# Kernel tuning notes

Measured on AMD Instinct MI355X. Metric: run time of the kernel, lower is better.

Reference implementation:

```python
import jax, jax.numpy as jnp
import numpy as np

N = 2048

def setup_inputs() -> dict:
    key = jax.random.key(0)
    k0, k1, k2, k3 = jax.random.split(key, 4)
    return {
        "input": jax.random.normal(k0, (N, N), dtype=jnp.float32),
        "weight1": jax.random.normal(k1, (N, N), dtype=jnp.float32),
        "weight2": jax.random.normal(k2, (N, N), dtype=jnp.float32),
        "weight3": jax.random.normal(k3, (N, N), dtype=jnp.float32),
    }

def reference(input, weight1, weight2, weight3):
    # Faithful translation of the torch DAG (duplicate mm kept: t4 == t2,
    # so t8 is mathematically zero, but we preserve the original math).
    t1 = input @ weight1
    t2 = input @ weight2
    t3 = weight3 @ weight3
    t4 = input @ weight2
    t5 = t1 * weight1
    t6 = (t5 @ input) * weight1
    t7 = t1 * t2 + t1 + t3
    t8 = t2 - t4
    t9 = t7 * t8 + t6 * t3
    t11 = t3 * t9
    t12 = t3 * (t1 @ input) * t6
    t13 = t7 + t11
    t14 = t8 + t12
    t15 = t13 + t14
    return t15
```

## Files before the change

### kernel.cpp

```cpp
#include <hip/hip_runtime.h>
#include <hip/hip_bf16.h>
#include <stdint.h>

#define NN 2048
#define BK 32
#define NK (NN / BK)

typedef __bf16 bf16;
typedef __bf16 bf16x8 __attribute__((ext_vector_type(8)));
typedef __bf16 bf16x4 __attribute__((ext_vector_type(4)));
typedef float f32x4 __attribute__((ext_vector_type(4)));

__device__ __forceinline__ void async_copy16(bf16* lds, const bf16* g) {
    __builtin_amdgcn_global_load_lds(
        (const __attribute__((address_space(1))) unsigned int*)g,
        (__attribute__((address_space(3))) unsigned int*)lds,
        16, 0, 0);
}

#define WAIT_VM(n) asm volatile("s_waitcnt vmcnt(" #n ")" ::: "memory")
#define LGKM0()    asm volatile("s_waitcnt lgkmcnt(0)" ::: "memory")
#define BAR()                                  \
    do {                                       \
        asm volatile("" ::: "memory");         \
        __builtin_amdgcn_s_barrier();          \
        asm volatile("" ::: "memory");         \
    } while (0)

struct CastArgs {
    const float* in[4];
    bf16*        outT[4];
    bf16*        outN[4];
};

__global__ __launch_bounds__(256) void transpose_cast_kernel(CastArgs args) {
    const float* __restrict__ in = args.in[blockIdx.z];
    bf16* __restrict__ outT      = args.outT[blockIdx.z];
    bf16* __restrict__ outN      = args.outN[blockIdx.z];
    __shared__ float tile[64][65];
    const int bx = blockIdx.x * 64;
    const int by = blockIdx.y * 64;
    const int t  = threadIdx.x;
    const int c4 = (t & 15) * 4, r0 = t >> 4;
#pragma unroll
    for (int p = 0; p < 4; ++p) {
        const int r = r0 + p * 16;
        const float4 v = *(const float4*)&in[(size_t)(by + r) * NN + bx + c4];
        tile[r][c4 + 0] = v.x; tile[r][c4 + 1] = v.y;
        tile[r][c4 + 2] = v.z; tile[r][c4 + 3] = v.w;
        if (outN) {
            bf16x4 b = {(bf16)v.x, (bf16)v.y, (bf16)v.z, (bf16)v.w};
            *(bf16x4*)&outN[(size_t)(by + r) * NN + bx + c4] = b;
        }
    }
    __syncthreads();
    const int cc8 = (t & 7) * 8, rw0 = t >> 3;
#pragma unroll
    for (int p = 0; p < 2; ++p) {
        const int rw = rw0 + p * 32;
        bf16x8 b;
#pragma unroll
        for (int i = 0; i < 8; ++i) b[i] = (bf16)tile[cc8 + i][rw];
        *(bf16x8*)&outT[(size_t)(bx + rw) * NN + by + cc8] = b;
    }
}

struct P1Args {
    const bf16*  Abf;
    const bf16*  W1t;
    const bf16*  W2t;
    const bf16*  W3bf;
    const bf16*  W3t;
    float*       M1;
    float*       M2out;
    float*       M3;
    const float* W1;
    bf16*        M1bf;
    bf16*        B1bf;
};

__global__ __launch_bounds__(512, 2) void gemm_dual_kernel(P1Args a) {
    __shared__ __align__(16) bf16 LA[4][128 * BK];
    __shared__ __align__(16) bf16 LB[4][128 * BK];
    __shared__ __align__(16) bf16 LC[4][128 * BK];

    const int t = threadIdx.x;
    const int wg  = blockIdx.y * 16 + blockIdx.x;
    const int swz = (wg & 7) * 32 + (wg >> 3);
    const int bm  = (swz >> 4) * 128;
    const int bn  = (swz & 15) * 128;

    const int srow = t >> 2;
    const int sch  = t & 3;
    const int scol = ((sch ^ ((srow >> 1) & 3)) << 3);
    const int off0 = t * 8;

    const int wave = t >> 6;
    const int lane = t & 63;
    const int lrow = lane & 15;
    const int q    = lane >> 4;
    const int qe   = (q ^ ((lrow >> 1) & 3)) << 3;

    if (blockIdx.z == 0) {
        const int wm = (wave >> 2) * 64;
        const int wn = (wave & 3) * 32;

        const bf16* gA  = a.Abf + (size_t)(bm + srow) * NN + scol;
        const bf16* gB1 = a.W1t + (size_t)(bn + srow) * NN + scol;
        const bf16* gB2 = a.W2t + (size_t)(bn + srow) * NN + scol;

        f32x4 acc1[4][2], acc2[4][2];
#pragma unroll
        for (int i = 0; i < 4; ++i)
#pragma unroll
            for (int j = 0; j < 2; ++j) {
                acc1[i][j] = (f32x4){0.f, 0.f, 0.f, 0.f};
                acc2[i][j] = (f32x4){0.f, 0.f, 0.f, 0.f};
            }

        auto issue = [&](int buf, int kt) {
            const int kof = kt * BK;
            async_copy16(&LA[buf][off0], gA  + kof);
            async_copy16(&LB[buf][off0], gB1 + kof);
            async_copy16(&LC[buf][off0], gB2 + kof);
        };

        issue(0, 0); issue(1, 1); issue(2, 2);
        WAIT_VM(6); BAR();

#pragma unroll 1
        for (int kt = 0; kt < NK; ++kt) {
            const int b = kt & 3;
            const bf16* cA = LA[b];
            const bf16* cB = LB[b];
            const bf16* cC = LC[b];

            bf16x8 af[4], f1[2], f2[2];
#pragma unroll
            for (int i = 0; i < 4; ++i)
                af[i] = *(const bf16x8*)&cA[(wm + i * 16 + lrow) * BK + qe];
#pragma unroll
            for (int j = 0; j < 2; ++j) {
                f1[j] = *(const bf16x8*)&cB[(wn + j * 16 + lrow) * BK + qe];
                f2[j] = *(const bf16x8*)&cC[(wn + j * 16 + lrow) * BK + qe];
            }
            if (kt < NK - 3) issue((kt + 3) & 3, kt + 3);

            BAR(); LGKM0();
            __builtin_amdgcn_s_setprio(1);
#pragma unroll
            for (int i = 0; i < 4; ++i)
#pragma unroll
                for (int j = 0; j < 2; ++j) {
                    acc1[i][j] = __builtin_amdgcn_mfma_f32_16x16x32_bf16(
                        af[i], f1[j], acc1[i][j], 0, 0, 0);
                    acc2[i][j] = __builtin_amdgcn_mfma_f32_16x16x32_bf16(
                        af[i], f2[j], acc2[i][j], 0, 0, 0);
                }
            __builtin_amdgcn_s_setprio(0);
            if (kt < NK - 3)       { WAIT_VM(6); }
            else if (kt == NK - 3) { WAIT_VM(3); }
            else                   { WAIT_VM(0); }
            BAR();
        }

#pragma unroll
        for (int i = 0; i < 4; ++i)
#pragma unroll
            for (int j = 0; j < 2; ++j)
#pragma unroll
                for (int r = 0; r < 4; ++r) {
                    const size_t idx =
                        (size_t)(bm + wm + i * 16 + q * 4 + r) * NN +
                        (bn + wn + j * 16 + lrow);
                    const float v1 = acc1[i][j][r];
                    a.M1[idx]    = v1;
                    a.M2out[idx] = acc2[i][j][r];
                    const float w = a.W1[idx];
                    a.M1bf[idx] = (bf16)v1;
                    a.B1bf[idx] = (bf16)(v1 * w);
                }
    } else {
        const int wm = (wave >> 2) * 64;
        const int wn = (wave & 3) * 32;

        const bf16* gA = a.W3bf + (size_t)(bm + srow) * NN + scol;
        const bf16* gB = a.W3t  + (size_t)(bn + srow) * NN + scol;

        f32x4 acc[4][2];
#pragma unroll
        for (int i = 0; i < 4; ++i)
#pragma unroll
            for (int j = 0; j < 2; ++j) acc[i][j] = (f32x4){0.f, 0.f, 0.f, 0.f};

        auto issue = [&](int buf, int kt) {
            const int kof = kt * BK;
            async_copy16(&LA[buf][off0], gA + kof);
            async_copy16(&LB[buf][off0], gB + kof);
        };

        issue(0, 0); issue(1, 1); issue(2, 2);
        WAIT_VM(4); BAR();

#pragma unroll 1
        for (int kt = 0; kt < NK; ++kt) {
            const int b = kt & 3;
            const bf16* cA = LA[b];
            const bf16* cB = LB[b];

            bf16x8 af[4], f1[2];
#pragma unroll
            for (int i = 0; i < 4; ++i)
                af[i] = *(const bf16x8*)&cA[(wm + i * 16 + lrow) * BK + qe];
#pragma unroll
            for (int j = 0; j < 2; ++j)
                f1[j] = *(const bf16x8*)&cB[(wn + j * 16 + lrow) * BK + qe];
            if (kt < NK - 3) issue((kt + 3) & 3, kt + 3);

            BAR(); LGKM0();
            __builtin_amdgcn_s_setprio(1);
#pragma unroll
            for (int i = 0; i < 4; ++i)
#pragma unroll
                for (int j = 0; j < 2; ++j)
                    acc[i][j] = __builtin_amdgcn_mfma_f32_16x16x32_bf16(
                        af[i], f1[j], acc[i][j], 0, 0, 0);
            __builtin_amdgcn_s_setprio(0);
            if (kt < NK - 3)       { WAIT_VM(4); }
            else if (kt == NK - 3) { WAIT_VM(2); }
            else                   { WAIT_VM(0); }
            BAR();
        }

#pragma unroll
        for (int i = 0; i < 4; ++i)
#pragma unroll
            for (int j = 0; j < 2; ++j)
#pragma unroll
                for (int r = 0; r < 4; ++r)
                    a.M3[(size_t)(bm + wm + i * 16 + q * 4 + r) * NN +
                         (bn + wn + j * 16 + lrow)] = acc[i][j][r];
    }
}

struct Gemm2Args {
    const bf16*  M1bf;
    const bf16*  B1bf;
    const bf16*  At;
    const float* M1;
    const float* M3;
    const float* W1;
    float*       out;
};

__global__ __launch_bounds__(512, 2) void gemm2_fused_kernel(Gemm2Args a) {
    __shared__ __align__(16) bf16 L5[4][128 * BK];
    __shared__ __align__(16) bf16 L4[4][128 * BK];
    __shared__ __align__(16) bf16 LBt[4][128 * BK];

    const int t = threadIdx.x;
    const int wg  = blockIdx.y * 16 + blockIdx.x;
    const int swz = (wg & 7) * 32 + (wg >> 3);
    const int bm  = (swz >> 4) * 128;
    const int bn  = (swz & 15) * 128;

    const int srow = t >> 2;
    const int sch  = t & 3;
    const int scol = ((sch ^ ((srow >> 1) & 3)) << 3);
    const int off0 = t * 8;

    const int wave = t >> 6;
    const int lane = t & 63;
    const int wm   = (wave >> 1) * 32;
    const int wn   = (wave & 1) * 64;
    const int lrow = lane & 15;
    const int q    = lane >> 4;
    const int qe   = (q ^ ((lrow >> 1) & 3)) << 3;

    const bf16* g5 = a.M1bf + (size_t)(bm + srow) * NN + scol;
    const bf16* g4 = a.B1bf + (size_t)(bm + srow) * NN + scol;
    const bf16* gB = a.At   + (size_t)(bn + srow) * NN + scol;

    f32x4 acc5[2][4], acc4[2][4];
#pragma unroll
    for (int i = 0; i < 2; ++i)
#pragma unroll
        for (int j = 0; j < 4; ++j) {
            acc5[i][j] = (f32x4){0.f, 0.f, 0.f, 0.f};
            acc4[i][j] = (f32x4){0.f, 0.f, 0.f, 0.f};
        }

    auto issue = [&](int buf, int kt) {
        const int kof = kt * BK;
        async_copy16(&L5[buf][off0],  g5 + kof);
        async_copy16(&L4[buf][off0],  g4 + kof);
        async_copy16(&LBt[buf][off0], gB + kof);
    };

    issue(0, 0); issue(1, 1); issue(2, 2);
    WAIT_VM(6); BAR();

#pragma unroll 1
    for (int kt = 0; kt < NK; ++kt) {
        const int b = kt & 3;
        const bf16* c5 = L5[b];
        const bf16* c4 = L4[b];
        const bf16* cB = LBt[b];

        bf16x8 a5[2], a4[2], bfr[4];
#pragma unroll
        for (int i = 0; i < 2; ++i) {
            a5[i] = *(const bf16x8*)&c5[(wm + i * 16 + lrow) * BK + qe];
            a4[i] = *(const bf16x8*)&c4[(wm + i * 16 + lrow) * BK + qe];
        }
#pragma unroll
        for (int j = 0; j < 4; ++j)
            bfr[j] = *(const bf16x8*)&cB[(wn + j * 16 + lrow) * BK + qe];
        if (kt < NK - 3) issue((kt + 3) & 3, kt + 3);

        BAR(); LGKM0();
        __builtin_amdgcn_s_setprio(1);
#pragma unroll
        for (int i = 0; i < 2; ++i)
#pragma unroll
            for (int j = 0; j < 4; ++j) {
                acc5[i][j] = __builtin_amdgcn_mfma_f32_16x16x32_bf16(
                    a5[i], bfr[j], acc5[i][j], 0, 0, 0);
                acc4[i][j] = __builtin_amdgcn_mfma_f32_16x16x32_bf16(
                    a4[i], bfr[j], acc4[i][j], 0, 0, 0);
            }
        __builtin_amdgcn_s_setprio(0);
        if (kt < NK - 3)       { WAIT_VM(6); }
        else if (kt == NK - 3) { WAIT_VM(3); }
        else                   { WAIT_VM(0); }
        BAR();
    }

#pragma unroll
    for (int i = 0; i < 2; ++i)
#pragma unroll
        for (int j = 0; j < 4; ++j)
#pragma unroll
            for (int r = 0; r < 4; ++r) {
                const size_t idx = (size_t)(bm + wm + i * 16 + q * 4 + r) * NN +
                                   (bn + wn + j * 16 + lrow);
                const float m5 = acc5[i][j][r];
                const float m4 = acc4[i][j][r];
                const float m1 = a.M1[idx];
                const float m3 = a.M3[idx];
                const float w1 = a.W1[idx];
                const float m2 = a.out[idx];
                a.out[idx] = m1 * m2 + m1 + m3 + m3 * (m4 * w1) * (m3 + m5);
            }
}

extern "C" void kernel_launch(void* const* d_in, const int* in_sizes, int n_in,
                              void* d_out, int out_size, void* d_ws, size_t ws_size,
                              hipStream_t stream) {
    const float* A  = (const float*)d_in[0];
    const float* W1 = (const float*)d_in[1];
    const float* W2 = (const float*)d_in[2];
    const float* W3 = (const float*)d_in[3];
    float* out = (float*)d_out;

    const size_t P = (size_t)NN * NN;
    char* ws = (char*)d_ws;

    bf16* Abf  = (bf16*)ws;
    bf16* At   = Abf + P;
    bf16* W1t  = At + P;
    bf16* W2t  = W1t + P;
    bf16* W3bf = W2t + P;
    bf16* W3t  = W3bf + P;
    bf16* M1bf = W3t + P;
    bf16* B1bf = M1bf + P;
    float* M1  = (float*)(B1bf + P);
    float* M3  = M1 + P;

    CastArgs ca;
    ca.in[0] = A;  ca.outT[0] = At;  ca.outN[0] = Abf;
    ca.in[1] = W1; ca.outT[1] = W1t; ca.outN[1] = nullptr;
    ca.in[2] = W2; ca.outT[2] = W2t; ca.outN[2] = nullptr;
    ca.in[3] = W3; ca.outT[3] = W3t; ca.outN[3] = W3bf;
    transpose_cast_kernel<<<dim3(NN / 64, NN / 64, 4), 256, 0, stream>>>(ca);

    P1Args p1;
    p1.Abf = Abf; p1.W1t = W1t; p1.W2t = W2t; p1.W3bf = W3bf; p1.W3t = W3t;
    p1.M1 = M1; p1.M2out = out; p1.M3 = M3;
    p1.W1 = W1; p1.M1bf = M1bf; p1.B1bf = B1bf;
    gemm_dual_kernel<<<dim3(NN / 128, NN / 128, 2), 512, 0, stream>>>(p1);

    Gemm2Args g2;
    g2.M1bf = M1bf; g2.B1bf = B1bf; g2.At = At;
    g2.M1 = M1; g2.M3 = M3; g2.W1 = W1; g2.out = out;
    gemm2_fused_kernel<<<dim3(NN / 128, NN / 128), 512, 0, stream>>>(g2);
}
```

Baseline: 237.2 us.

## Halve threads per block with 64x64 warp tiles and triple-buffered single-barrier pipeline

Both GEMM kernels move from 512 to 256 threads per block. Each wave now computes a 64x64 sub-tile, so it holds more accumulators and reuses each LDS fragment more often. The LDS ring shrinks from 4 to 3 stages with a prefetch distance of 2, and each thread issues two async copies per matrix. The per-iteration barrier plus lgkmcnt wait is removed, leaving one barrier per iteration. This cuts LDS read traffic and synchronization per MFMA, but it raises register pressure (up to 128 accumulator floats per thread), may lower occupancy, and gives less latency hiding from the shallower pipeline.

```diff
diff --git a/kernel.cpp b/kernel.cpp
--- a/kernel.cpp
+++ b/kernel.cpp
@@ -19,7 +19,6 @@
 }
 
 #define WAIT_VM(n) asm volatile("s_waitcnt vmcnt(" #n ")" ::: "memory")
-#define LGKM0()    asm volatile("s_waitcnt lgkmcnt(0)" ::: "memory")
 #define BAR()                                  \
     do {                                       \
         asm volatile("" ::: "memory");         \
@@ -79,10 +78,10 @@
     bf16*        B1bf;
 };
 
-__global__ __launch_bounds__(512, 2) void gemm_dual_kernel(P1Args a) {
-    __shared__ __align__(16) bf16 LA[4][128 * BK];
-    __shared__ __align__(16) bf16 LB[4][128 * BK];
-    __shared__ __align__(16) bf16 LC[4][128 * BK];
+__global__ __launch_bounds__(256, 2) void gemm_dual_kernel(P1Args a) {
+    __shared__ __align__(16) bf16 LA[3][128 * BK];
+    __shared__ __align__(16) bf16 LB[3][128 * BK];
+    __shared__ __align__(16) bf16 LC[3][128 * BK];
 
     const int t = threadIdx.x;
     const int wg  = blockIdx.y * 16 + blockIdx.x;
@@ -97,77 +96,77 @@
 
     const int wave = t >> 6;
     const int lane = t & 63;
+    const int wm   = (wave >> 1) * 64;
+    const int wn   = (wave & 1) * 64;
     const int lrow = lane & 15;
     const int q    = lane >> 4;
     const int qe   = (q ^ ((lrow >> 1) & 3)) << 3;
 
     if (blockIdx.z == 0) {
-        const int wm = (wave >> 2) * 64;
-        const int wn = (wave & 3) * 32;
-
         const bf16* gA  = a.Abf + (size_t)(bm + srow) * NN + scol;
         const bf16* gB1 = a.W1t + (size_t)(bn + srow) * NN + scol;
         const bf16* gB2 = a.W2t + (size_t)(bn + srow) * NN + scol;
 
-        f32x4 acc1[4][2], acc2[4][2];
-#pragma unroll
-        for (int i = 0; i < 4; ++i)
-#pragma unroll
-            for (int j = 0; j < 2; ++j) {
+        f32x4 acc1[4][4], acc2[4][4];
+#pragma unroll
+        for (int i = 0; i < 4; ++i)
+#pragma unroll
+            for (int j = 0; j < 4; ++j) {
                 acc1[i][j] = (f32x4){0.f, 0.f, 0.f, 0.f};
                 acc2[i][j] = (f32x4){0.f, 0.f, 0.f, 0.f};
             }
 
         auto issue = [&](int buf, int kt) {
             const int kof = kt * BK;
-            async_copy16(&LA[buf][off0], gA  + kof);
-            async_copy16(&LB[buf][off0], gB1 + kof);
-            async_copy16(&LC[buf][off0], gB2 + kof);
+            async_copy16(&LA[buf][off0],           gA  + kof);
+            async_copy16(&LA[buf][off0 + 64 * BK], gA  + (size_t)64 * NN + kof);
+            async_copy16(&LB[buf][off0],           gB1 + kof);
+            async_copy16(&LB[buf][off0 + 64 * BK], gB1 + (size_t)64 * NN + kof);
+            async_copy16(&LC[buf][off0],           gB2 + kof);
+            async_copy16(&LC[buf][off0 + 64 * BK], gB2 + (size_t)64 * NN + kof);
         };
 
-        issue(0, 0); issue(1, 1); issue(2, 2);
+        issue(0, 0); issue(1, 1);
         WAIT_VM(6); BAR();
 
 #pragma unroll 1
         for (int kt = 0; kt < NK; ++kt) {
-            const int b = kt & 3;
+            const int b = kt % 3;
+            if (kt < NK - 2) issue((kt + 2) % 3, kt + 2);
+
             const bf16* cA = LA[b];
             const bf16* cB = LB[b];
             const bf16* cC = LC[b];
-
-            bf16x8 af[4], f1[2], f2[2];
+            bf16x8 af[4], f1[4], f2[4];
 #pragma unroll
             for (int i = 0; i < 4; ++i)
                 af[i] = *(const bf16x8*)&cA[(wm + i * 16 + lrow) * BK + qe];
 #pragma unroll
-            for (int j = 0; j < 2; ++j) {
+            for (int j = 0; j < 4; ++j) {
                 f1[j] = *(const bf16x8*)&cB[(wn + j * 16 + lrow) * BK + qe];
                 f2[j] = *(const bf16x8*)&cC[(wn + j * 16 + lrow) * BK + qe];
             }
-            if (kt < NK - 3) issue((kt + 3) & 3, kt + 3);
-
-            BAR(); LGKM0();
+
             __builtin_amdgcn_s_setprio(1);
 #pragma unroll
             for (int i = 0; i < 4; ++i)
 #pragma unroll
-                for (int j = 0; j < 2; ++j) {
+                for (int j = 0; j < 4; ++j) {
                     acc1[i][j] = __builtin_amdgcn_mfma_f32_16x16x32_bf16(
                         af[i], f1[j], acc1[i][j], 0, 0, 0);
                     acc2[i][j] = __builtin_amdgcn_mfma_f32_16x16x32_bf16(
                         af[i], f2[j], acc2[i][j], 0, 0, 0);
                 }
             __builtin_amdgcn_s_setprio(0);
-            if (kt < NK - 3)       { WAIT_VM(6); }
-            else if (kt == NK - 3) { WAIT_VM(3); }
-            else                   { WAIT_VM(0); }
-            BAR();
-        }
-
-#pragma unroll
-        for (int i = 0; i < 4; ++i)
-#pragma unroll
-            for (int j = 0; j < 2; ++j)
+
+            if (kt < NK - 2)       { WAIT_VM(6); BAR(); }
+            else if (kt == NK - 2) { WAIT_VM(0); BAR(); }
+        }
+
+#pragma unroll
+        for (int i = 0; i < 4; ++i)
+#pragma unroll
+            for (int j = 0; j < 4; ++j)
 #pragma unroll
                 for (int r = 0; r < 4; ++r) {
                     const size_t idx =
@@ -181,61 +180,58 @@
                     a.B1bf[idx] = (bf16)(v1 * w);
                 }
     } else {
-        const int wm = (wave >> 2) * 64;
-        const int wn = (wave & 3) * 32;
-
         const bf16* gA = a.W3bf + (size_t)(bm + srow) * NN + scol;
         const bf16* gB = a.W3t  + (size_t)(bn + srow) * NN + scol;
 
-        f32x4 acc[4][2];
-#pragma unroll
-        for (int i = 0; i < 4; ++i)
-#pragma unroll
-            for (int j = 0; j < 2; ++j) acc[i][j] = (f32x4){0.f, 0.f, 0.f, 0.f};
+        f32x4 acc[4][4];
+#pragma unroll
+        for (int i = 0; i < 4; ++i)
+#pragma unroll
+            for (int j = 0; j < 4; ++j) acc[i][j] = (f32x4){0.f, 0.f, 0.f, 0.f};
 
         auto issue = [&](int buf, int kt) {
             const int kof = kt * BK;
-            async_copy16(&LA[buf][off0], gA + kof);
-            async_copy16(&LB[buf][off0], gB + kof);
+            async_copy16(&LA[buf][off0],           gA + kof);
+            async_copy16(&LA[buf][off0 + 64 * BK], gA + (size_t)64 * NN + kof);
+            async_copy16(&LB[buf][off0],           gB + kof);
+            async_copy16(&LB[buf][off0 + 64 * BK], gB + (size_t)64 * NN + kof);
         };
 
-        issue(0, 0); issue(1, 1); issue(2, 2);
+        issue(0, 0); issue(1, 1);
         WAIT_VM(4); BAR();
 
 #pragma unroll 1
         for (int kt = 0; kt < NK; ++kt) {
-            const int b = kt & 3;
+            const int b = kt % 3;
+            if (kt < NK - 2) issue((kt + 2) % 3, kt + 2);
+
             const bf16* cA = LA[b];
             const bf16* cB = LB[b];
-
-            bf16x8 af[4], f1[2];
+            bf16x8 af[4], f1[4];
 #pragma unroll
             for (int i = 0; i < 4; ++i)
                 af[i] = *(const bf16x8*)&cA[(wm + i * 16 + lrow) * BK + qe];
 #pragma unroll
-            for (int j = 0; j < 2; ++j)
+            for (int j = 0; j < 4; ++j)
                 f1[j] = *(const bf16x8*)&cB[(wn + j * 16 + lrow) * BK + qe];
-            if (kt < NK - 3) issue((kt + 3) & 3, kt + 3);
-
-            BAR(); LGKM0();
+
             __builtin_amdgcn_s_setprio(1);
 #pragma unroll
             for (int i = 0; i < 4; ++i)
 #pragma unroll
-                for (int j = 0; j < 2; ++j)
+                for (int j = 0; j < 4; ++j)
                     acc[i][j] = __builtin_amdgcn_mfma_f32_16x16x32_bf16(
                         af[i], f1[j], acc[i][j], 0, 0, 0);
             __builtin_amdgcn_s_setprio(0);
-            if (kt < NK - 3)       { WAIT_VM(4); }
-            else if (kt == NK - 3) { WAIT_VM(2); }
-            else                   { WAIT_VM(0); }
-            BAR();
-        }
-
-#pragma unroll
-        for (int i = 0; i < 4; ++i)
-#pragma unroll
-            for (int j = 0; j < 2; ++j)
+
+            if (kt < NK - 2)       { WAIT_VM(4); BAR(); }
+            else if (kt == NK - 2) { WAIT_VM(0); BAR(); }
+        }
+
+#pragma unroll
+        for (int i = 0; i < 4; ++i)
+#pragma unroll
+            for (int j = 0; j < 4; ++j)
 #pragma unroll
                 for (int r = 0; r < 4; ++r)
                     a.M3[(size_t)(bm + wm + i * 16 + q * 4 + r) * NN +
@@ -253,10 +249,10 @@
     float*       out;
 };
 
-__global__ __launch_bounds__(512, 2) void gemm2_fused_kernel(Gemm2Args a) {
-    __shared__ __align__(16) bf16 L5[4][128 * BK];
-    __shared__ __align__(16) bf16 L4[4][128 * BK];
-    __shared__ __align__(16) bf16 LBt[4][128 * BK];
+__global__ __launch_bounds__(256, 2) void gemm2_fused_kernel(Gemm2Args a) {
+    __shared__ __align__(16) bf16 L5[3][128 * BK];
+    __shared__ __align__(16) bf16 L4[3][128 * BK];
+    __shared__ __align__(16) bf16 LBt[3][128 * BK];
 
     const int t = threadIdx.x;
     const int wg  = blockIdx.y * 16 + blockIdx.x;
@@ -271,7 +267,7 @@
 
     const int wave = t >> 6;
     const int lane = t & 63;
-    const int wm   = (wave >> 1) * 32;
+    const int wm   = (wave >> 1) * 64;
     const int wn   = (wave & 1) * 64;
     const int lrow = lane & 15;
     const int q    = lane >> 4;
@@ -281,9 +277,9 @@
     const bf16* g4 = a.B1bf + (size_t)(bm + srow) * NN + scol;
     const bf16* gB = a.At   + (size_t)(bn + srow) * NN + scol;
 
-    f32x4 acc5[2][4], acc4[2][4];
-#pragma unroll
-    for (int i = 0; i < 2; ++i)
+    f32x4 acc5[4][4], acc4[4][4];
+#pragma unroll
+    for (int i = 0; i < 4; ++i)
 #pragma unroll
         for (int j = 0; j < 4; ++j) {
             acc5[i][j] = (f32x4){0.f, 0.f, 0.f, 0.f};
@@ -292,36 +288,38 @@
 
     auto issue = [&](int buf, int kt) {
         const int kof = kt * BK;
-        async_copy16(&L5[buf][off0],  g5 + kof);
-        async_copy16(&L4[buf][off0],  g4 + kof);
-        async_copy16(&LBt[buf][off0], gB + kof);
+        async_copy16(&L5[buf][off0],            g5 + kof);
+        async_copy16(&L5[buf][off0 + 64 * BK],  g5 + (size_t)64 * NN + kof);
+        async_copy16(&L4[buf][off0],            g4 + kof);
+        async_copy16(&L4[buf][off0 + 64 * BK],  g4 + (size_t)64 * NN + kof);
+        async_copy16(&LBt[buf][off0],           gB + kof);
+        async_copy16(&LBt[buf][off0 + 64 * BK], gB + (size_t)64 * NN + kof);
     };
 
-    issue(0, 0); issue(1, 1); issue(2, 2);
+    issue(0, 0); issue(1, 1);
     WAIT_VM(6); BAR();
 
 #pragma unroll 1
     for (int kt = 0; kt < NK; ++kt) {
-        const int b = kt & 3;
+        const int b = kt % 3;
+        if (kt < NK - 2) issue((kt + 2) % 3, kt + 2);
+
         const bf16* c5 = L5[b];
         const bf16* c4 = L4[b];
         const bf16* cB = LBt[b];
-
-        bf16x8 a5[2], a4[2], bfr[4];
-#pragma unroll
-        for (int i = 0; i < 2; ++i) {
+        bf16x8 a5[4], a4[4], bfr[4];
+#pragma unroll
+        for (int i = 0; i < 4; ++i) {
             a5[i] = *(const bf16x8*)&c5[(wm + i * 16 + lrow) * BK + qe];
             a4[i] = *(const bf16x8*)&c4[(wm + i * 16 + lrow) * BK + qe];
         }
 #pragma unroll
         for (int j = 0; j < 4; ++j)
             bfr[j] = *(const bf16x8*)&cB[(wn + j * 16 + lrow) * BK + qe];
-        if (kt < NK - 3) issue((kt + 3) & 3, kt + 3);
-
-        BAR(); LGKM0();
+
         __builtin_amdgcn_s_setprio(1);
 #pragma unroll
-        for (int i = 0; i < 2; ++i)
+        for (int i = 0; i < 4; ++i)
 #pragma unroll
             for (int j = 0; j < 4; ++j) {
                 acc5[i][j] = __builtin_amdgcn_mfma_f32_16x16x32_bf16(
@@ -330,14 +328,13 @@
                     a4[i], bfr[j], acc4[i][j], 0, 0, 0);
             }
         __builtin_amdgcn_s_setprio(0);
-        if (kt < NK - 3)       { WAIT_VM(6); }
-        else if (kt == NK - 3) { WAIT_VM(3); }
-        else                   { WAIT_VM(0); }
-        BAR();
+
+        if (kt < NK - 2)       { WAIT_VM(6); BAR(); }
+        else if (kt == NK - 2) { WAIT_VM(0); BAR(); }
     }
 
 #pragma unroll
-    for (int i = 0; i < 2; ++i)
+    for (int i = 0; i < 4; ++i)
 #pragma unroll
         for (int j = 0; j < 4; ++j)
 #pragma unroll
@@ -388,10 +385,10 @@
     p1.Abf = Abf; p1.W1t = W1t; p1.W2t = W2t; p1.W3bf = W3bf; p1.W3t = W3t;
     p1.M1 = M1; p1.M2out = out; p1.M3 = M3;
     p1.W1 = W1; p1.M1bf = M1bf; p1.B1bf = B1bf;
-    gemm_dual_kernel<<<dim3(NN / 128, NN / 128, 2), 512, 0, stream>>>(p1);
+    gemm_dual_kernel<<<dim3(NN / 128, NN / 128, 2), 256, 0, stream>>>(p1);
 
     Gemm2Args g2;
     g2.M1bf = M1bf; g2.B1bf = B1bf; g2.At = At;
     g2.M1 = M1; g2.M3 = M3; g2.W1 = W1; g2.out = out;
-    gemm2_fused_kernel<<<dim3(NN / 128, NN / 128), 512, 0, stream>>>(g2);
-}
+    gemm2_fused_kernel<<<dim3(NN / 128, NN / 128), 256, 0, stream>>>(g2);
+}
```

Result: slower. 264.9 us (+11.7%).
